# Optimization experiments

Hardware: AMD Instinct MI355X
Metric: run time of the kernel (lower is better)

## Reference

```python
import jax, jax.numpy as jnp
import numpy as np

K_HARRIS = 0.04

def _conv3x3(x, ker):
    # x: [B,1,H,W], ker: [1,1,3,3]; cross-correlation w/ padding 1 (matches torch F.conv2d)
    return jax.lax.conv_general_dilated(
        x, ker, window_strides=(1, 1), padding=((1, 1), (1, 1)),
        dimension_numbers=("NCHW", "OIHW", "NCHW"))


def setup_inputs() -> dict:
    key = jax.random.key(0)
    x = jax.random.normal(key, (16, 3, 1024, 1024), dtype=jnp.float32)
    return {"x": x, "k": 512, "patch_size": 5}


def reference(x, k, patch_size):
    B, C, H, W = x.shape
    dt = x.dtype
    margin = patch_size
    mask = jnp.zeros((H, W), dt).at[margin:H - margin, margin:W - margin].set(1.0)

    img = jnp.mean(x, axis=1, keepdims=True) if C != 1 else x  # [B,1,H,W]

    kx = jnp.array([[[[-1, 0, 1], [-1, 0, 1], [-1, 0, 1]]]], dt)
    ky = jnp.array([[[[-1, -1, -1], [0, 0, 0], [1, 1, 1]]]], dt)
    dx = _conv3x3(img, kx)
    dy = _conv3x3(img, ky)

    g = (jnp.array([[1, 2, 1], [2, 4, 2], [1, 2, 1]], dt) / 16.0)[None, None]
    Sxx = _conv3x3(dx * dx, g)
    Syy = _conv3x3(dy * dy, g)
    Sxy = _conv3x3(dx * dy, g)

    det = Sxx * Syy - Sxy ** 2
    trace = Sxx + Syy
    R = (det - K_HARRIS * trace ** 2).squeeze(1) * mask  # [B,H,W]

    _, idx = jax.lax.top_k(R.reshape(B, H * W), k)  # [B,k]
    coords = jnp.stack([idx // W, idx % W], axis=-1).astype(dt)  # [B,k,2] (row,col)
    coords = (coords / jnp.array([H, W], dt) - 0.5) * 2.0
    return jnp.clip(coords.reshape(B, k, 2), -1.0, 1.0)
```

## Files before the change

kernel.cpp:

```cpp
#include <hip/hip_runtime.h>
#include <stdint.h>

#define HH 1024
#define WW 1024
#define NB 16
#define KTOP 512
#define NBINS 4096
#define CAP 8192
#define ROWS 16

typedef unsigned long long u64;
typedef unsigned int u32;

__device__ __forceinline__ u32 fmap(float v) {
    u32 u = __float_as_uint(v);
    return (u & 0x80000000u) ? ~u : (u | 0x80000000u);
}
__device__ __forceinline__ float fadd(float a, float b){ return __fadd_rn(a,b); }
__device__ __forceinline__ float fsub(float a, float b){ return __fsub_rn(a,b); }
__device__ __forceinline__ float fmul(float a, float b){ return __fmul_rn(a,b); }
__device__ __forceinline__ float add3(float a, float b, float c){ return fadd(fadd(a,b),c); }
__device__ __forceinline__ float mean3(float a, float b, float c){
    return __fdiv_rn(add3(a,b,c), 3.0f);
}

__device__ __forceinline__ float g9(float w00,float w01,float w02,
                                    float w10,float w11,float w12,
                                    float w20,float w21,float w22){
    float s = fadd(w00, fmul(2.0f,w01));
    s = fadd(s, w02);
    s = fadd(s, fmul(2.0f,w10));
    s = fadd(s, fmul(4.0f,w11));
    s = fadd(s, fmul(2.0f,w12));
    s = fadd(s, w20);
    s = fadd(s, fmul(2.0f,w21));
    s = fadd(s, w22);
    return fmul(s, 0.0625f);
}
__device__ __forceinline__ u32 respkey(float Sxx,float Syy,float Sxy,bool masked){
    float det = fsub(fmul(Sxx,Syy), fmul(Sxy,Sxy));
    float tr  = fadd(Sxx,Syy);
    float R   = fsub(det, fmul(fmul(0.04f,tr),tr));
    if (masked) R = 0.0f;
    return fmap(R);
}

__device__ __forceinline__ float4 vmean(float4 a, float4 b, float4 c){
    return make_float4(mean3(a.x,b.x,c.x), mean3(a.y,b.y,c.y),
                       mean3(a.z,b.z,c.z), mean3(a.w,b.w,c.w));
}
__device__ __forceinline__ float4 vadd3(float4 a, float4 b, float4 c){
    return make_float4(add3(a.x,b.x,c.x), add3(a.y,b.y,c.y),
                       add3(a.z,b.z,c.z), add3(a.w,b.w,c.w));
}
__device__ __forceinline__ float4 vsub(float4 a, float4 b){
    return make_float4(fsub(a.x,b.x), fsub(a.y,b.y), fsub(a.z,b.z), fsub(a.w,b.w));
}
__device__ __forceinline__ float4 vmul(float4 a, float4 b){
    return make_float4(fmul(a.x,b.x), fmul(a.y,b.y), fmul(a.z,b.z), fmul(a.w,b.w));
}
__device__ __forceinline__ float4 shl1(float4 v, float edge, int lane){
    float w = __shfl_up(v.w, 1);
    if (lane == 0) w = edge;
    return make_float4(w, v.x, v.y, v.z);
}
__device__ __forceinline__ float4 shr1(float4 v, float edge, int lane){
    float e = __shfl_down(v.x, 1);
    if (lane == 63) e = edge;
    return make_float4(v.y, v.z, v.w, e);
}

__global__ __launch_bounds__(256) void harris_a(const float* __restrict__ x,
                                                u32* __restrict__ gmax) {
    const int b     = blockIdx.y;
    const int task  = blockIdx.x * 4 + (threadIdx.x >> 6);
    const int lane  = threadIdx.x & 63;
    const int strip = task & 3;
    const int y0    = (task >> 2) * ROWS;
    const int sx    = strip * 256;
    const int cx    = sx + 4 * lane;
    const int hx    = (lane < 32) ? max(sx - 4, 0) : min(sx + 256, WW - 4);
    const float* p0 = x + (size_t)b * 3 * HH * WW;
    const float* p1 = p0 + HH * WW;
    const float* p2 = p1 + HH * WW;

    float4 z4 = make_float4(0.f,0.f,0.f,0.f);
    float4 m0=z4,m1=z4,m2=z4, mh0=z4,mh1=z4,mh2=z4, h0=z4,h1=z4,h2=z4;
    float he0=0.f,he1=0.f,he2=0.f;
    float4 xx0=z4,xx1=z4,xx2=z4, yy0=z4,yy1=z4,yy2=z4, xy0=z4,xy1=z4,xy2=z4;
    float exx0=0.f,exx1=0.f,exx2=0.f, eyy0=0.f,eyy1=0.f,eyy2=0.f, exy0=0.f,exy1=0.f,exy2=0.f;

    #pragma unroll
    for (int t = 0; t < ROWS + 4; ++t) {
        m0=m1; m1=m2; mh0=mh1; mh1=mh2; h0=h1; h1=h2; he0=he1; he1=he2;
        int ym = min(max(y0 - 2 + t, 0), HH - 1);
        size_t ro = (size_t)ym * WW;
        float4 a0 = *(const float4*)(p0 + ro + cx);
        float4 a1 = *(const float4*)(p1 + ro + cx);
        float4 a2 = *(const float4*)(p2 + ro + cx);
        m2 = vmean(a0, a1, a2);
        float4 b0 = *(const float4*)(p0 + ro + hx);
        float4 b1 = *(const float4*)(p1 + ro + hx);
        float4 b2 = *(const float4*)(p2 + ro + hx);
        mh2 = vmean(b0, b1, b2);
        float4 m2l = shl1(m2, mh2.w, lane);
        float4 m2r = shr1(m2, mh2.x, lane);
        h2  = vadd3(m2l, m2, m2r);
        he2 = (lane < 32) ? add3(mh2.z, mh2.w, m2.x) : add3(m2.w, mh2.x, mh2.y);

        if (t >= 2) {
            xx0=xx1; xx1=xx2; yy0=yy1; yy1=yy2; xy0=xy1; xy1=xy2;
            exx0=exx1; exx1=exx2; eyy0=eyy1; eyy1=eyy2; exy0=exy1; exy1=exy2;
            float4 s  = vadd3(m0, m1, m2);
            float4 sh = vadd3(mh0, mh1, mh2);
            float4 sl = shl1(s, sh.w, lane);
            float4 sr = shr1(s, sh.x, lane);
            float4 dx = vsub(sr, sl);
            float4 dy = vsub(h2, h0);
            xx2 = vmul(dx, dx); yy2 = vmul(dy, dy); xy2 = vmul(dx, dy);
            float dxe = (lane < 32) ? fsub(s.x, sh.z) : fsub(sh.y, s.w);
            float dye = fsub(he2, he0);
            exx2 = fmul(dxe, dxe); eyy2 = fmul(dye, dye); exy2 = fmul(dxe, dye);
        }
        if (t >= 4) {
            int y = y0 + t - 4;
            bool rowm = (y < 5) || (y > HH - 6);
            float4 xxl0 = shl1(xx0, exx0, lane), xxr0 = shr1(xx0, exx0, lane);
            float4 xxl1 = shl1(xx1, exx1, lane), xxr1 = shr1(xx1, exx1, lane);
            float4 xxl2 = shl1(xx2, exx2, lane), xxr2 = shr1(xx2, exx2, lane);
            float4 yyl0 = shl1(yy0, eyy0, lane), yyr0 = shr1(yy0, eyy0, lane);
            float4 yyl1 = shl1(yy1, eyy1, lane), yyr1 = shr1(yy1, eyy1, lane);
            float4 yyl2 = shl1(yy2, eyy2, lane), yyr2 = shr1(yy2, eyy2, lane);
            float4 xyl0 = shl1(xy0, exy0, lane), xyr0 = shr1(xy0, exy0, lane);
            float4 xyl1 = shl1(xy1, exy1, lane), xyr1 = shr1(xy1, exy1, lane);
            float4 xyl2 = shl1(xy2, exy2, lane), xyr2 = shr1(xy2, exy2, lane);

            u32 k[4];
            {
                float Sxx, Syy, Sxy; int gx; bool mk;
                Sxx = g9(xxl0.x,xx0.x,xxr0.x, xxl1.x,xx1.x,xxr1.x, xxl2.x,xx2.x,xxr2.x);
                Syy = g9(yyl0.x,yy0.x,yyr0.x, yyl1.x,yy1.x,yyr1.x, yyl2.x,yy2.x,yyr2.x);
                Sxy = g9(xyl0.x,xy0.x,xyr0.x, xyl1.x,xy1.x,xyr1.x, xyl2.x,xy2.x,xyr2.x);
                gx = cx + 0; mk = rowm || (gx < 5) || (gx > WW - 6);
                k[0] = respkey(Sxx, Syy, Sxy, mk);
                Sxx = g9(xxl0.y,xx0.y,xxr0.y, xxl1.y,xx1.y,xxr1.y, xxl2.y,xx2.y,xxr2.y);
                Syy = g9(yyl0.y,yy0.y,yyr0.y, yyl1.y,yy1.y,yyr1.y, yyl2.y,yy2.y,yyr2.y);
                Sxy = g9(xyl0.y,xy0.y,xyr0.y, xyl1.y,xy1.y,xyr1.y, xyl2.y,xy2.y,xyr2.y);
                gx = cx + 1; mk = rowm || (gx < 5) || (gx > WW - 6);
                k[1] = respkey(Sxx, Syy, Sxy, mk);
                Sxx = g9(xxl0.z,xx0.z,xxr0.z, xxl1.z,xx1.z,xxr1.z, xxl2.z,xx2.z,xxr2.z);
                Syy = g9(yyl0.z,yy0.z,yyr0.z, yyl1.z,yy1.z,yyr1.z, yyl2.z,yy2.z,yyr2.z);
                Sxy = g9(xyl0.z,xy0.z,xyr0.z, xyl1.z,xy1.z,xyr1.z, xyl2.z,xy2.z,xyr2.z);
                gx = cx + 2; mk = rowm || (gx < 5) || (gx > WW - 6);
                k[2] = respkey(Sxx, Syy, Sxy, mk);
                Sxx = g9(xxl0.w,xx0.w,xxr0.w, xxl1.w,xx1.w,xxr1.w, xxl2.w,xx2.w,xxr2.w);
                Syy = g9(yyl0.w,yy0.w,yyr0.w, yyl1.w,yy1.w,yyr1.w, yyl2.w,yy2.w,yyr2.w);
                Sxy = g9(xyl0.w,xy0.w,xyr0.w, xyl1.w,xy1.w,xyr1.w, xyl2.w,xy2.w,xyr2.w);
                gx = cx + 3; mk = rowm || (gx < 5) || (gx > WW - 6);
                k[3] = respkey(Sxx, Syy, Sxy, mk);
            }
            u32 km = max(max(k[0], k[1]), max(k[2], k[3]));
            #pragma unroll
            for (int off = 1; off < 16; off <<= 1)
                km = max(km, (u32)__shfl_xor((int)km, off));
            if ((lane & 15) == 0)
                gmax[((size_t)b << 14) | ((size_t)y << 4) | (u32)(strip * 4 + (lane >> 4))] = km;
        }
    }
}

__global__ __launch_bounds__(512) void select_b(const u32* __restrict__ gmax,
                                                u32* __restrict__ glist,
                                                u32* __restrict__ gcount,
                                                u32* __restrict__ cutb) {
    __shared__ u32 hist[NBINS];
    __shared__ u32 wsum[8];
    __shared__ u32 s_cut, s_n;
    const int b = blockIdx.x;
    const int tid = threadIdx.x;
    const u32* gm = gmax + ((size_t)b << 14);
    u32 val[32];
    #pragma unroll
    for (int j = 0; j < 8; ++j) {
        uint4 v = ((const uint4*)gm)[tid + j * 512];
        val[j*4+0]=v.x; val[j*4+1]=v.y; val[j*4+2]=v.z; val[j*4+3]=v.w;
    }
    for (int i = tid; i < NBINS; i += 512) hist[i] = 0u;
    if (tid == 0) s_n = 0u;
    __syncthreads();
    #pragma unroll
    for (int j = 0; j < 32; ++j) atomicAdd(&hist[val[j] >> 20], 1u);
    __syncthreads();
    u32 lv[8], ls = 0;
    #pragma unroll
    for (int i = 0; i < 8; ++i) { lv[i] = hist[tid*8+i]; ls += lv[i]; }
    const int lane = tid & 63, w = tid >> 6;
    u32 v = ls;
    #pragma unroll
    for (int off = 1; off < 64; off <<= 1) {
        u32 t2 = (u32)__shfl_down((int)v, off);
        if (lane + off < 64) v += t2;
    }
    if (lane == 0) wsum[w] = v;
    __syncthreads();
    u32 excl = v - ls;
    #pragma unroll
    for (int i = 0; i < 8; ++i) if (i > w) excl += wsum[i];
    if (excl < KTOP && excl + ls >= KTOP) {
        u32 acc = excl;
        #pragma unroll
        for (int i = 7; i >= 0; --i) {
            acc += lv[i];
            if (acc >= KTOP) { s_cut = (u32)(tid*8 + i); break; }
        }
    }
    __syncthreads();
    const u32 cut = s_cut;
    u32* gl = glist + ((size_t)b << 14);
    #pragma unroll
    for (int j = 0; j < 8; ++j)
        #pragma unroll
        for (int kk = 0; kk < 4; ++kk) {
            u32 gv = val[j*4+kk];
            if ((gv >> 20) >= cut) {
                u32 q = atomicAdd(&s_n, 1u);
                gl[q] = (u32)(j*2048 + 4*tid + kk);
            }
        }
    __syncthreads();
    if (tid == 0) { gcount[b] = s_n; cutb[b] = cut; }
}

__device__ __forceinline__ u32 harris_px(const float* __restrict__ p0,
                                         const float* __restrict__ p1,
                                         const float* __restrict__ p2,
                                         int gy, int gx) {
    if (gy < 5 || gy > HH - 6 || gx < 5 || gx > WW - 6) return 0x80000000u;
    float m[5][5];
    #pragma unroll
    for (int r = 0; r < 5; ++r)
        #pragma unroll
        for (int c = 0; c < 5; ++c) {
            size_t o = (size_t)(gy - 2 + r) * WW + (gx - 2 + c);
            m[r][c] = mean3(p0[o], p1[o], p2[o]);
        }
    float pxx[3][3], pyy[3][3], pxy[3][3];
    #pragma unroll
    for (int pr = 0; pr < 3; ++pr) {
        float s[5], ht[3], hb[3];
        #pragma unroll
        for (int c = 0; c < 5; ++c) s[c] = add3(m[pr][c], m[pr+1][c], m[pr+2][c]);
        #pragma unroll
        for (int c = 0; c < 3; ++c) {
            ht[c] = add3(m[pr][c],   m[pr][c+1],   m[pr][c+2]);
            hb[c] = add3(m[pr+2][c], m[pr+2][c+1], m[pr+2][c+2]);
        }
        #pragma unroll
        for (int pc = 0; pc < 3; ++pc) {
            float dx = fsub(s[pc+2], s[pc]);
            float dy = fsub(hb[pc], ht[pc]);
            pxx[pr][pc] = fmul(dx, dx);
            pyy[pr][pc] = fmul(dy, dy);
            pxy[pr][pc] = fmul(dx, dy);
        }
    }
    float Sxx = g9(pxx[0][0],pxx[0][1],pxx[0][2],pxx[1][0],pxx[1][1],pxx[1][2],pxx[2][0],pxx[2][1],pxx[2][2]);
    float Syy = g9(pyy[0][0],pyy[0][1],pyy[0][2],pyy[1][0],pyy[1][1],pyy[1][2],pyy[2][0],pyy[2][1],pyy[2][2]);
    float Sxy = g9(pxy[0][0],pxy[0][1],pxy[0][2],pxy[1][0],pxy[1][1],pxy[1][2],pxy[2][0],pxy[2][1],pxy[2][2]);
    return respkey(Sxx, Syy, Sxy, false);
}

__global__ __launch_bounds__(256) void refine_c(const float* __restrict__ x,
                                                const u32* __restrict__ glist,
                                                const u32* __restrict__ gcount,
                                                const u32* __restrict__ cutb,
                                                u32* __restrict__ cnt,
                                                u64* __restrict__ cand) {
    __shared__ u64 sbuf[CAP];
    __shared__ u32 s_n, s_base;
    const int b = blockIdx.y;
    const u32 gc  = gcount[b];
    const u32 cut = cutb[b];
    const int tid = threadIdx.x;
    const int wv = tid >> 6, lane = tid & 63;
    if (tid == 0) s_n = 0u;
    __syncthreads();

    const u32 per = (gc + 31) >> 5;
    const u32 i0  = blockIdx.x * per;
    const u32 i1  = min(i0 + per, gc);
    const float* p0 = x + (size_t)b * 3 * HH * WW;
    const float* p1 = p0 + HH * WW;
    const float* p2 = p1 + HH * WW;
    const u32* gl = glist + ((size_t)b << 14);

    for (u32 i = i0 + wv; i < i1; i += 4) {
        u32 gid = gl[i];
        int gy = (int)(gid >> 4);
        int gx = (int)((gid & 15u) << 6) + lane;
        u32 key = harris_px(p0, p1, p2, gy, gx);
        bool pred = (key >> 20) >= cut;
        u64 mball = __ballot(pred);
        if (mball) {
            int first = __ffsll((unsigned long long)mball) - 1;
            u32 base = 0;
            if (lane == first) base = atomicAdd(&s_n, (u32)__popcll(mball));
            base = __shfl(base, first);
            if (pred) {
                u32 q = base + (u32)__popcll(mball & ((1ull << lane) - 1));
                if (q < CAP) sbuf[q] = ((u64)key << 32) | (u32)~((u32)(gy << 10) | (u32)gx);
            }
        }
    }
    __syncthreads();
    u32 n = min(s_n, (u32)CAP);
    if (tid == 0) s_base = atomicAdd(&cnt[b * 16], n);
    __syncthreads();
    u32 gb = s_base;
    u64* cb = cand + (size_t)b * CAP;
    for (u32 j = tid; j < n; j += 256) {
        u32 q = gb + j;
        if (q < CAP) cb[q] = sbuf[j];
    }
}

__global__ __launch_bounds__(1024) void sort_d(const u32* __restrict__ cnt,
                                               const u64* __restrict__ cand,
                                               float* __restrict__ out) {
    __shared__ u64 s[CAP];
    const int b = blockIdx.x;
    u32 n = cnt[b * 16];
    if (n > CAP) n = CAP;
    u32 P = 512;
    while (P < n) P <<= 1;
    for (u32 i = threadIdx.x; i < P; i += 1024)
        s[i] = (i < n) ? cand[(size_t)b * CAP + i] : 0ULL;
    __syncthreads();
    for (u32 size = 2; size <= P; size <<= 1) {
        for (u32 stride = size >> 1; stride > 0; stride >>= 1) {
            for (u32 t = threadIdx.x; t < (P >> 1); t += 1024) {
                u32 i = 2 * t - (t & (stride - 1));
                u32 j = i + stride;
                u64 a = s[i], c = s[j];
                bool desc = ((i & size) == 0);
                if (desc ? (a < c) : (a > c)) { s[i] = c; s[j] = a; }
            }
            __syncthreads();
        }
    }
    if (threadIdx.x < KTOP) {
        u64 k = s[threadIdx.x];
        u32 idx = ~(u32)k;
        u32 row = idx >> 10, col = idx & 1023;
        float rf = ((float)row * (1.0f / 1024.0f) - 0.5f) * 2.0f;
        float cf = ((float)col * (1.0f / 1024.0f) - 0.5f) * 2.0f;
        rf = fminf(fmaxf(rf, -1.0f), 1.0f);
        cf = fminf(fmaxf(cf, -1.0f), 1.0f);
        float* o = out + ((size_t)b * KTOP + threadIdx.x) * 2;
        o[0] = rf;
        o[1] = cf;
    }
}

extern "C" void kernel_launch(void* const* d_in, const int* in_sizes, int n_in,
                              void* d_out, int out_size, void* d_ws, size_t ws_size,
                              hipStream_t stream) {
    const float* x = (const float*)d_in[0];
    float* out = (float*)d_out;
    char* ws = (char*)d_ws;

    u32* gmax   = (u32*)ws;
    u32* glist  = (u32*)(ws + (1u << 20));
    u32* gcount = (u32*)(ws + (2u << 20));
    u32* cutb   = (u32*)(ws + (2u << 20) + 64);
    u32* cnt    = (u32*)(ws + (2u << 20) + 128);
    u64* cand   = (u64*)(ws + (2u << 20) + 2048);

    hipMemsetAsync(cnt, 0, 1024, stream);
    hipLaunchKernelGGL(harris_a, dim3(64, NB), dim3(256), 0, stream, x, gmax);
    hipLaunchKernelGGL(select_b, dim3(NB), dim3(512), 0, stream, gmax, glist, gcount, cutb);
    hipLaunchKernelGGL(refine_c, dim3(32, NB), dim3(256), 0, stream, x, glist, gcount, cutb, cnt, cand);
    hipLaunchKernelGGL(sort_d, dim3(NB), dim3(1024), 0, stream, cnt, cand, out);
}
```

Baseline: 119.7 us.

## Cut shuffle and register pressure in Harris stencil, fold counter reset into select

```diff
diff --git a/kernel.cpp b/kernel.cpp
--- a/kernel.cpp
+++ b/kernel.cpp
@@ -53,25 +53,9 @@
     return make_float4(add3(a.x,b.x,c.x), add3(a.y,b.y,c.y),
                        add3(a.z,b.z,c.z), add3(a.w,b.w,c.w));
 }
-__device__ __forceinline__ float4 vsub(float4 a, float4 b){
-    return make_float4(fsub(a.x,b.x), fsub(a.y,b.y), fsub(a.z,b.z), fsub(a.w,b.w));
-}
-__device__ __forceinline__ float4 vmul(float4 a, float4 b){
-    return make_float4(fmul(a.x,b.x), fmul(a.y,b.y), fmul(a.z,b.z), fmul(a.w,b.w));
-}
-__device__ __forceinline__ float4 shl1(float4 v, float edge, int lane){
-    float w = __shfl_up(v.w, 1);
-    if (lane == 0) w = edge;
-    return make_float4(w, v.x, v.y, v.z);
-}
-__device__ __forceinline__ float4 shr1(float4 v, float edge, int lane){
-    float e = __shfl_down(v.x, 1);
-    if (lane == 63) e = edge;
-    return make_float4(v.y, v.z, v.w, e);
-}
-
-__global__ __launch_bounds__(256) void harris_a(const float* __restrict__ x,
-                                                u32* __restrict__ gmax) {
+
+__global__ __launch_bounds__(256, 4) void harris_a(const float* __restrict__ x,
+                                                   u32* __restrict__ gmax) {
     const int b     = blockIdx.y;
     const int task  = blockIdx.x * 4 + (threadIdx.x >> 6);
     const int lane  = threadIdx.x & 63;
@@ -80,19 +64,26 @@
     const int sx    = strip * 256;
     const int cx    = sx + 4 * lane;
     const int hx    = (lane < 32) ? max(sx - 4, 0) : min(sx + 256, WW - 4);
+    const bool lo32 = (lane < 32);
     const float* p0 = x + (size_t)b * 3 * HH * WW;
     const float* p1 = p0 + HH * WW;
     const float* p2 = p1 + HH * WW;
 
     float4 z4 = make_float4(0.f,0.f,0.f,0.f);
-    float4 m0=z4,m1=z4,m2=z4, mh0=z4,mh1=z4,mh2=z4, h0=z4,h1=z4,h2=z4;
+    float4 m0=z4, m1=z4, m2=z4, h0=z4, h1=z4, h2=z4;
+    float hma0=0.f,hma1=0.f,hma2=0.f, hmb0=0.f,hmb1=0.f,hmb2=0.f;
     float he0=0.f,he1=0.f,he2=0.f;
-    float4 xx0=z4,xx1=z4,xx2=z4, yy0=z4,yy1=z4,yy2=z4, xy0=z4,xy1=z4,xy2=z4;
-    float exx0=0.f,exx1=0.f,exx2=0.f, eyy0=0.f,eyy1=0.f,eyy2=0.f, exy0=0.f,exy1=0.f,exy2=0.f;
+    float PXX[3][6], PYY[3][6], PXY[3][6];
+    #pragma unroll
+    for (int r = 0; r < 3; ++r)
+        #pragma unroll
+        for (int i = 0; i < 6; ++i) { PXX[r][i]=0.f; PYY[r][i]=0.f; PXY[r][i]=0.f; }
 
     #pragma unroll
     for (int t = 0; t < ROWS + 4; ++t) {
-        m0=m1; m1=m2; mh0=mh1; mh1=mh2; h0=h1; h1=h2; he0=he1; he1=he2;
+        m0=m1; m1=m2; h0=h1; h1=h2;
+        hma0=hma1; hma1=hma2; hmb0=hmb1; hmb1=hmb2;
+        he0=he1; he1=he2;
         int ym = min(max(y0 - 2 + t, 0), HH - 1);
         size_t ro = (size_t)ym * WW;
         float4 a0 = *(const float4*)(p0 + ro + cx);
@@ -102,62 +93,82 @@
         float4 b0 = *(const float4*)(p0 + ro + hx);
         float4 b1 = *(const float4*)(p1 + ro + hx);
         float4 b2 = *(const float4*)(p2 + ro + hx);
-        mh2 = vmean(b0, b1, b2);
-        float4 m2l = shl1(m2, mh2.w, lane);
-        float4 m2r = shr1(m2, mh2.x, lane);
-        h2  = vadd3(m2l, m2, m2r);
-        he2 = (lane < 32) ? add3(mh2.z, mh2.w, m2.x) : add3(m2.w, mh2.x, mh2.y);
+        {
+            float ca0 = lo32 ? b0.z : b0.x, ca1 = lo32 ? b1.z : b1.x, ca2 = lo32 ? b2.z : b2.x;
+            float cb0 = lo32 ? b0.w : b0.y, cb1 = lo32 ? b1.w : b1.y, cb2 = lo32 ? b2.w : b2.y;
+            hma2 = mean3(ca0, ca1, ca2);
+            hmb2 = mean3(cb0, cb1, cb2);
+        }
+        {
+            float upw = __shfl_up(m2.w, 1);
+            float dnx = __shfl_down(m2.x, 1);
+            float lm  = (lane == 0)  ? hmb2 : upw;
+            float rm  = (lane == 63) ? hma2 : dnx;
+            h2 = make_float4(add3(lm,   m2.x, m2.y),
+                             add3(m2.x, m2.y, m2.z),
+                             add3(m2.y, m2.z, m2.w),
+                             add3(m2.z, m2.w, rm));
+            he2 = lo32 ? add3(hma2, hmb2, m2.x) : add3(m2.w, hma2, hmb2);
+        }
 
         if (t >= 2) {
-            xx0=xx1; xx1=xx2; yy0=yy1; yy1=yy2; xy0=xy1; xy1=xy2;
-            exx0=exx1; exx1=exx2; eyy0=eyy1; eyy1=eyy2; exy0=exy1; exy1=exy2;
-            float4 s  = vadd3(m0, m1, m2);
-            float4 sh = vadd3(mh0, mh1, mh2);
-            float4 sl = shl1(s, sh.w, lane);
-            float4 sr = shr1(s, sh.x, lane);
-            float4 dx = vsub(sr, sl);
-            float4 dy = vsub(h2, h0);
-            xx2 = vmul(dx, dx); yy2 = vmul(dy, dy); xy2 = vmul(dx, dy);
-            float dxe = (lane < 32) ? fsub(s.x, sh.z) : fsub(sh.y, s.w);
+            #pragma unroll
+            for (int i = 0; i < 6; ++i) {
+                PXX[0][i]=PXX[1][i]; PXX[1][i]=PXX[2][i];
+                PYY[0][i]=PYY[1][i]; PYY[1][i]=PYY[2][i];
+                PXY[0][i]=PXY[1][i]; PXY[1][i]=PXY[2][i];
+            }
+            float4 s = vadd3(m0, m1, m2);
+            float sva = add3(hma0, hma1, hma2);
+            float svb = add3(hmb0, hmb1, hmb2);
+            float upsw = __shfl_up(s.w, 1);
+            float dnsx = __shfl_down(s.x, 1);
+            float sm1 = (lane == 0)  ? svb : upsw;
+            float sp4 = (lane == 63) ? sva : dnsx;
+            float dx0 = fsub(s.y, sm1);
+            float dx1 = fsub(s.z, s.x);
+            float dx2 = fsub(s.w, s.y);
+            float dx3 = fsub(sp4, s.z);
+            float updx = __shfl_up(dx3, 1);
+            float dndx = __shfl_down(dx0, 1);
+            float dxm1 = (lane == 0)  ? fsub(s.x, sva) : updx;
+            float dxp4 = (lane == 63) ? fsub(svb, s.w) : dndx;
+            float dy0 = fsub(h2.x, h0.x);
+            float dy1 = fsub(h2.y, h0.y);
+            float dy2 = fsub(h2.z, h0.z);
+            float dy3 = fsub(h2.w, h0.w);
             float dye = fsub(he2, he0);
-            exx2 = fmul(dxe, dxe); eyy2 = fmul(dye, dye); exy2 = fmul(dxe, dye);
+            float updy = __shfl_up(dy3, 1);
+            float dndy = __shfl_down(dy0, 1);
+            float dym1 = (lane == 0)  ? dye : updy;
+            float dyp4 = (lane == 63) ? dye : dndy;
+            float DX[6] = {dxm1, dx0, dx1, dx2, dx3, dxp4};
+            float DY[6] = {dym1, dy0, dy1, dy2, dy3, dyp4};
+            #pragma unroll
+            for (int i = 0; i < 6; ++i) {
+                PXX[2][i] = fmul(DX[i], DX[i]);
+                PYY[2][i] = fmul(DY[i], DY[i]);
+                PXY[2][i] = fmul(DX[i], DY[i]);
+            }
         }
         if (t >= 4) {
             int y = y0 + t - 4;
             bool rowm = (y < 5) || (y > HH - 6);
-            float4 xxl0 = shl1(xx0, exx0, lane), xxr0 = shr1(xx0, exx0, lane);
-            float4 xxl1 = shl1(xx1, exx1, lane), xxr1 = shr1(xx1, exx1, lane);
-            float4 xxl2 = shl1(xx2, exx2, lane), xxr2 = shr1(xx2, exx2, lane);
-            float4 yyl0 = shl1(yy0, eyy0, lane), yyr0 = shr1(yy0, eyy0, lane);
-            float4 yyl1 = shl1(yy1, eyy1, lane), yyr1 = shr1(yy1, eyy1, lane);
-            float4 yyl2 = shl1(yy2, eyy2, lane), yyr2 = shr1(yy2, eyy2, lane);
-            float4 xyl0 = shl1(xy0, exy0, lane), xyr0 = shr1(xy0, exy0, lane);
-            float4 xyl1 = shl1(xy1, exy1, lane), xyr1 = shr1(xy1, exy1, lane);
-            float4 xyl2 = shl1(xy2, exy2, lane), xyr2 = shr1(xy2, exy2, lane);
-
             u32 k[4];
-            {
-                float Sxx, Syy, Sxy; int gx; bool mk;
-                Sxx = g9(xxl0.x,xx0.x,xxr0.x, xxl1.x,xx1.x,xxr1.x, xxl2.x,xx2.x,xxr2.x);
-                Syy = g9(yyl0.x,yy0.x,yyr0.x, yyl1.x,yy1.x,yyr1.x, yyl2.x,yy2.x,yyr2.x);
-                Sxy = g9(xyl0.x,xy0.x,xyr0.x, xyl1.x,xy1.x,xyr1.x, xyl2.x,xy2.x,xyr2.x);
-                gx = cx + 0; mk = rowm || (gx < 5) || (gx > WW - 6);
-                k[0] = respkey(Sxx, Syy, Sxy, mk);
-                Sxx = g9(xxl0.y,xx0.y,xxr0.y, xxl1.y,xx1.y,xxr1.y, xxl2.y,xx2.y,xxr2.y);
-                Syy = g9(yyl0.y,yy0.y,yyr0.y, yyl1.y,yy1.y,yyr1.y, yyl2.y,yy2.y,yyr2.y);
-                Sxy = g9(xyl0.y,xy0.y,xyr0.y, xyl1.y,xy1.y,xyr1.y, xyl2.y,xy2.y,xyr2.y);
-                gx = cx + 1; mk = rowm || (gx < 5) || (gx > WW - 6);
-                k[1] = respkey(Sxx, Syy, Sxy, mk);
-                Sxx = g9(xxl0.z,xx0.z,xxr0.z, xxl1.z,xx1.z,xxr1.z, xxl2.z,xx2.z,xxr2.z);
-                Syy = g9(yyl0.z,yy0.z,yyr0.z, yyl1.z,yy1.z,yyr1.z, yyl2.z,yy2.z,yyr2.z);
-                Sxy = g9(xyl0.z,xy0.z,xyr0.z, xyl1.z,xy1.z,xyr1.z, xyl2.z,xy2.z,xyr2.z);
-                gx = cx + 2; mk = rowm || (gx < 5) || (gx > WW - 6);
-                k[2] = respkey(Sxx, Syy, Sxy, mk);
-                Sxx = g9(xxl0.w,xx0.w,xxr0.w, xxl1.w,xx1.w,xxr1.w, xxl2.w,xx2.w,xxr2.w);
-                Syy = g9(yyl0.w,yy0.w,yyr0.w, yyl1.w,yy1.w,yyr1.w, yyl2.w,yy2.w,yyr2.w);
-                Sxy = g9(xyl0.w,xy0.w,xyr0.w, xyl1.w,xy1.w,xyr1.w, xyl2.w,xy2.w,xyr2.w);
-                gx = cx + 3; mk = rowm || (gx < 5) || (gx > WW - 6);
-                k[3] = respkey(Sxx, Syy, Sxy, mk);
+            #pragma unroll
+            for (int j = 0; j < 4; ++j) {
+                float Sxx = g9(PXX[0][j],PXX[0][j+1],PXX[0][j+2],
+                               PXX[1][j],PXX[1][j+1],PXX[1][j+2],
+                               PXX[2][j],PXX[2][j+1],PXX[2][j+2]);
+                float Syy = g9(PYY[0][j],PYY[0][j+1],PYY[0][j+2],
+                               PYY[1][j],PYY[1][j+1],PYY[1][j+2],
+                               PYY[2][j],PYY[2][j+1],PYY[2][j+2]);
+                float Sxy = g9(PXY[0][j],PXY[0][j+1],PXY[0][j+2],
+                               PXY[1][j],PXY[1][j+1],PXY[1][j+2],
+                               PXY[2][j],PXY[2][j+1],PXY[2][j+2]);
+                int gx = cx + j;
+                bool mk = rowm || (gx < 5) || (gx > WW - 6);
+                k[j] = respkey(Sxx, Syy, Sxy, mk);
             }
             u32 km = max(max(k[0], k[1]), max(k[2], k[3]));
             #pragma unroll
@@ -172,7 +183,8 @@
 __global__ __launch_bounds__(512) void select_b(const u32* __restrict__ gmax,
                                                 u32* __restrict__ glist,
                                                 u32* __restrict__ gcount,
-                                                u32* __restrict__ cutb) {
+                                                u32* __restrict__ cutb,
+                                                u32* __restrict__ cnt) {
     __shared__ u32 hist[NBINS];
     __shared__ u32 wsum[8];
     __shared__ u32 s_cut, s_n;
@@ -186,7 +198,7 @@
         val[j*4+0]=v.x; val[j*4+1]=v.y; val[j*4+2]=v.z; val[j*4+3]=v.w;
     }
     for (int i = tid; i < NBINS; i += 512) hist[i] = 0u;
-    if (tid == 0) s_n = 0u;
+    if (tid == 0) { s_n = 0u; cnt[b * 16] = 0u; }
     __syncthreads();
     #pragma unroll
     for (int j = 0; j < 32; ++j) atomicAdd(&hist[val[j] >> 20], 1u);
@@ -376,9 +388,8 @@
     u32* cnt    = (u32*)(ws + (2u << 20) + 128);
     u64* cand   = (u64*)(ws + (2u << 20) + 2048);
 
-    hipMemsetAsync(cnt, 0, 1024, stream);
     hipLaunchKernelGGL(harris_a, dim3(64, NB), dim3(256), 0, stream, x, gmax);
-    hipLaunchKernelGGL(select_b, dim3(NB), dim3(512), 0, stream, gmax, glist, gcount, cutb);
+    hipLaunchKernelGGL(select_b, dim3(NB), dim3(512), 0, stream, gmax, glist, gcount, cutb, cnt);
     hipLaunchKernelGGL(refine_c, dim3(32, NB), dim3(256), 0, stream, x, glist, gcount, cutb, cnt, cand);
     hipLaunchKernelGGL(sort_d, dim3(NB), dim3(1024), 0, stream, cnt, cand, out);
 }
```

After: 137.2 us. 1.15x slower.
